# Kernel tuning notes

Hardware: AMD Instinct MI355X
Metric: run time of the kernel (lower is better)

The kernel has to match this reference:

```python
import jax, jax.numpy as jnp
import numpy as np

N_NODE = 100000
EMB = 112
NNZ = 1000000
B = 512
L = 50
LAYERS = 2


def setup_inputs() -> dict:
    key = jax.random.key(0)
    ks = jax.random.split(key, 9)
    embedding = jax.random.normal(ks[0], (N_NODE, EMB), dtype=jnp.float32) * 0.1
    adj_vals = jax.random.uniform(ks[1], (NNZ,), dtype=jnp.float32)
    adj_rows = jax.random.randint(ks[2], (NNZ,), 0, N_NODE, dtype=jnp.int32)
    adj_cols = jax.random.randint(ks[3], (NNZ,), 0, N_NODE, dtype=jnp.int32)
    D = jax.random.normal(ks[4], (B, B), dtype=jnp.float32) * (1.0 / B)
    A = jax.random.normal(ks[5], (B, B), dtype=jnp.float32)
    session_item = jax.random.randint(ks[6], (B, L), 0, N_NODE + 1, dtype=jnp.int32)  # 0 = pad row
    session_len = jnp.floor(jax.random.uniform(ks[7], (B, 1), dtype=jnp.float32) * (L - 1)) + 1.0
    stdv = 1.0 / np.sqrt(EMB)
    w_sess = jax.random.normal(ks[8], (LAYERS, EMB, EMB), dtype=jnp.float32) * stdv
    return {"embedding": embedding, "adj_vals": adj_vals, "adj_rows": adj_rows,
            "adj_cols": adj_cols, "D": D, "A": A, "session_item": session_item,
            "session_len": session_len, "w_sess": w_sess}


def _l2_normalize(x, eps=1e-12):
    n = jnp.linalg.norm(x, axis=-1, keepdims=True)
    return x / jnp.maximum(n, eps)


def _hyperconv(embedding, adj_vals, adj_rows, adj_cols):
    # mean over layer outputs of repeated sparse.mm(adjacency, embedding)
    cur = embedding
    acc = embedding
    for _ in range(LAYERS):
        msgs = adj_vals[:, None] * cur[adj_cols]           # [nnz, E] gather
        cur = jax.ops.segment_sum(msgs, adj_rows, num_segments=N_NODE)
        acc = acc + cur
    return acc / (LAYERS + 1)


def _sessconv(item_emb, D, A, session_item, session_len, w_sess):
    pad_emb = jnp.concatenate([jnp.zeros((1, EMB), item_emb.dtype), item_emb], axis=0)
    seq_h = pad_emb[session_item]                           # [B, L, E] gather (vectorized index_select loop)
    sess = jnp.sum(seq_h, axis=1) / session_len             # [B, E] mean pool
    DA = D @ A                                              # [B, B]
    acc = sess
    for i in range(LAYERS):
        sess = sess @ w_sess[i].T                           # Linear, no bias
        sess = DA @ sess
        sess = _l2_normalize(sess)
        acc = acc + sess
    return acc / (LAYERS + 1)


def reference(embedding, adj_vals, adj_rows, adj_cols, D, A, session_item, session_len, w_sess):
    item_emb = _hyperconv(embedding, adj_vals, adj_rows, adj_cols)
    sess_emb = _sessconv(item_emb, D, A, session_item, session_len, w_sess)
    return sess_emb
```

## Files before the change

### kernel.cpp

```cpp
#include <hip/hip_runtime.h>
#include <hip/hip_bf16.h>

#define N_NODE 100000
#define EMB 112
#define EMBQ 28
#define EMBQ4 14
#define EMBP4 16
#define EMBP2 32
#define NNZ 1000000
#define BATCH 512
#define SEQL 50

typedef unsigned int uint32;

__device__ __forceinline__ unsigned short f2bf(float f) {
    uint32 u = __float_as_uint(f);
    u = (u + 0x7fffu + ((u >> 16) & 1u)) >> 16;
    return (unsigned short)u;
}
__device__ __forceinline__ uint32 pack_bf2(float x, float y) {
    return (uint32)f2bf(x) | ((uint32)f2bf(y) << 16);
}
__device__ __forceinline__ float2 unpack_bf2(uint32 p) {
    float2 r;
    r.x = __uint_as_float(p << 16);
    r.y = __uint_as_float(p & 0xffff0000u);
    return r;
}

#define NPAD 100352
#define NBUCKET 196
#define BCAP 6144
#define CHUNK 2048
#define MS_BLOCKS 489
#define MAXC 25600
#define POISON ((int)0xAAAAAAAA)

__global__ __launch_bounds__(256)
void split_prep_kernel(const int* __restrict__ rows,
                       const int* __restrict__ cols,
                       const float* __restrict__ vals,
                       int* __restrict__ cur, int2* __restrict__ tmp,
                       const float4* __restrict__ embf4,
                       uint2* __restrict__ embb2,
                       const int* __restrict__ items,
                       int* __restrict__ flags, int* __restrict__ mapv,
                       int* __restrict__ rlist, int* __restrict__ cntp) {
    __shared__ int hist[NBUCKET];
    __shared__ int lexcl[NBUCKET];
    __shared__ int gbase[NBUCKET];
    __shared__ int lcur[NBUCKET];
    __shared__ int sscan[256];
    __shared__ unsigned char sbuck[CHUNK];
    __shared__ int2 stage[CHUNK];
    int t = threadIdx.x;
    if (blockIdx.x < MS_BLOCKS) {
        int base = blockIdx.x * CHUNK;
        int m = NNZ - base; if (m > CHUNK) m = CHUNK;
        for (int j = t; j < NBUCKET; j += 256) hist[j] = 0;
        __syncthreads();
        for (int i = t; i < m; i += 256) atomicAdd(&hist[rows[base + i] >> 9], 1);
        __syncthreads();
        int v = (t < NBUCKET) ? hist[t] : 0;
        sscan[t] = v;
        __syncthreads();
#pragma unroll
        for (int d = 1; d < 256; d <<= 1) {
            int x = (t >= d) ? sscan[t - d] : 0;
            __syncthreads();
            sscan[t] += x;
            __syncthreads();
        }
        if (t < NBUCKET) {
            int e = sscan[t] - v;
            lexcl[t] = e;
            lcur[t] = e;
            gbase[t] = t * BCAP + (atomicAdd(&cur[t], v) - POISON);
        }
        __syncthreads();
        for (int i = t; i < m; i += 256) {
            int r = rows[base + i];
            int b = r >> 9;
            int p = atomicAdd(&lcur[b], 1);
            stage[p] = make_int2(cols[base + i] | ((r & 511) << 17),
                                 __float_as_int(vals[base + i]));
            sbuck[p] = (unsigned char)b;
        }
        __syncthreads();
        for (int i = t; i < m; i += 256) {
            int b = sbuck[i];
            tmp[gbase[b] + (i - lexcl[b])] = stage[i];
        }
    } else {
        int i = (blockIdx.x - MS_BLOCKS) * 256 + t;
        if (i < N_NODE * EMBP2) {
            int row = i >> 5, u = i & 31;
            uint2 o;
            if (u < EMBQ) {
                float4 v = embf4[row * EMBQ + u];
                o.x = pack_bf2(v.x, v.y);
                o.y = pack_bf2(v.z, v.w);
            } else {
                o.x = 0u;
                o.y = 0u;
            }
            embb2[i] = o;
        }
        if (i < BATCH * SEQL) {
            int it = items[i];
            if (it > 0) {
                int old = atomicCAS(&flags[it - 1], POISON, 1);
                if (old == POISON) {
                    int rank = atomicAdd(cntp, 1) - POISON;
                    mapv[it - 1] = rank;
                    rlist[rank] = it - 1;
                }
            }
        }
    }
}

__global__ __launch_bounds__(256)
void sort_gemm_kernel(const int* __restrict__ cur, const int2* __restrict__ tmp,
                      int2* __restrict__ edges, int* __restrict__ off,
                      const float* __restrict__ D, const float* __restrict__ A,
                      float* __restrict__ DA) {
    __shared__ __align__(16) char smem[56320];
    int t = threadIdx.x;
    if (blockIdx.x < NBUCKET) {
        int* hist   = (int*)smem;
        int* scanb  = (int*)(smem + 2048);
        int* lcur   = (int*)(smem + 4096);
        int* sscan  = (int*)(smem + 6144);
        int2* stage = (int2*)(smem + 7168);
        int b = blockIdx.x;
        int base = b * BCAP;
        int cnt = cur[b] - POISON;
        for (int j = t; j < 512; j += 256) hist[j] = 0;
        __syncthreads();
        for (int i = t; i < cnt; i += 256) {
            int2 e = tmp[base + i];
            stage[i] = e;
            atomicAdd(&hist[(e.x >> 17) & 511], 1);
        }
        __syncthreads();
        int a0 = hist[2 * t], a1 = hist[2 * t + 1];
        int s = a0 + a1;
        sscan[t] = s;
        __syncthreads();
#pragma unroll
        for (int d = 1; d < 256; d <<= 1) {
            int x = (t >= d) ? sscan[t - d] : 0;
            __syncthreads();
            sscan[t] += x;
            __syncthreads();
        }
        int excl = sscan[t] - s;
        scanb[2 * t] = excl;
        scanb[2 * t + 1] = excl + a0;
        lcur[2 * t] = excl;
        lcur[2 * t + 1] = excl + a0;
        __syncthreads();
        for (int j = t; j < 512; j += 256) off[(b << 9) + j] = base + scanb[j];
        for (int i = t; i < cnt; i += 256) {
            int2 e = stage[i];
            int rl = (e.x >> 17) & 511;
            int p = atomicAdd(&lcur[rl], 1);
            edges[base + p] = make_int2(e.x & 0x1FFFF, e.y);
        }
    } else {
        float (*sDt)[36] = (float(*)[36])smem;
        float (*sA)[68] = (float(*)[68])(smem + 2304);
        int bx = blockIdx.x - NBUCKET;
        int tx = t & 15, ty = t >> 4;
        int m0 = (bx >> 3) * 32, n0 = (bx & 7) * 64;
        float acc[2][4];
#pragma unroll
        for (int i = 0; i < 2; ++i)
#pragma unroll
            for (int j = 0; j < 4; ++j) acc[i][j] = 0.0f;
        int dm = t >> 2, dk = (t & 3) * 4;
        int ak = t >> 4, an = (t & 15) * 4;
        for (int k0 = 0; k0 < BATCH; k0 += 16) {
            float4 dv;
            if (t < 128)
                dv = *(const float4*)(D + (size_t)(m0 + dm) * BATCH + k0 + dk);
            float4 av = *(const float4*)(A + (size_t)(k0 + ak) * BATCH + n0 + an);
            __syncthreads();
            if (t < 128) {
                sDt[dk + 0][dm] = dv.x;
                sDt[dk + 1][dm] = dv.y;
                sDt[dk + 2][dm] = dv.z;
                sDt[dk + 3][dm] = dv.w;
            }
            *(float4*)&sA[ak][an] = av;
            __syncthreads();
#pragma unroll
            for (int k = 0; k < 16; ++k) {
                float a0 = sDt[k][ty * 2 + 0];
                float a1 = sDt[k][ty * 2 + 1];
                float4 bv = *(const float4*)&sA[k][tx * 4];
                float br[4] = {bv.x, bv.y, bv.z, bv.w};
#pragma unroll
                for (int j = 0; j < 4; ++j) {
                    acc[0][j] += a0 * br[j];
                    acc[1][j] += a1 * br[j];
                }
            }
        }
#pragma unroll
        for (int i = 0; i < 2; ++i) {
            float4 o = make_float4(acc[i][0], acc[i][1], acc[i][2], acc[i][3]);
            *(float4*)(DA + (size_t)(m0 + ty * 2 + i) * BATCH + n0 + tx * 4) = o;
        }
    }
}

__global__ __launch_bounds__(256, 8)
void spmm_csr_kernel(const uint32* __restrict__ curb,
                     const float4* __restrict__ embf,
                     const int* __restrict__ rowptr,
                     const int* __restrict__ bcnt,
                     const int2* __restrict__ edges,
                     const int* __restrict__ rlist,
                     const int* __restrict__ cntp,
                     void* __restrict__ outm, int fuse_final) {
    int t = threadIdx.x;
    int lane16 = t & 15;
    int slot = t >> 4;
    int srcbase = t & 48;
    int idx = (blockIdx.x << 4) + slot;
    int r;
    if (rlist) {
        if (idx >= cntp[0] - POISON) return;
        r = rlist[idx];
    } else {
        r = idx;
        if (r >= N_NODE) return;
    }
    int beg = rowptr[r];
    int end = ((r & 511) == 511) ? ((r >> 9) * BCAP + (bcnt[r >> 9] - POISON))
                                 : rowptr[r + 1];
    int len = end - beg;
    int q = lane16;
    const uint4* basep = (const uint4*)curb;
    float4 accA = make_float4(0.0f, 0.0f, 0.0f, 0.0f);
    float4 accB = make_float4(0.0f, 0.0f, 0.0f, 0.0f);
    for (int b0 = 0; b0 < len; b0 += 16) {
        int m = len - b0; if (m > 16) m = 16;
        int2 e = (lane16 < m) ? edges[beg + b0 + lane16] : make_int2(0, 0);
        for (int k = 0; k < m; k += 4) {
            int   c0 = __shfl(e.x, srcbase + k + 0, 64);
            float v0 = __int_as_float(__shfl(e.y, srcbase + k + 0, 64));
            int   c1 = __shfl(e.x, srcbase + k + 1, 64);
            float v1 = __int_as_float(__shfl(e.y, srcbase + k + 1, 64));
            int   c2 = __shfl(e.x, srcbase + k + 2, 64);
            float v2 = __int_as_float(__shfl(e.y, srcbase + k + 2, 64));
            int   c3 = __shfl(e.x, srcbase + k + 3, 64);
            float v3 = __int_as_float(__shfl(e.y, srcbase + k + 3, 64));
            uint4 x0 = basep[(c0 << 4) + q];
            uint4 x1 = basep[(c1 << 4) + q];
            uint4 x2 = basep[(c2 << 4) + q];
            uint4 x3 = basep[(c3 << 4) + q];
            float2 p0a = unpack_bf2(x0.x), p0b = unpack_bf2(x0.y),
                   p0c = unpack_bf2(x0.z), p0d = unpack_bf2(x0.w);
            float2 p1a = unpack_bf2(x1.x), p1b = unpack_bf2(x1.y),
                   p1c = unpack_bf2(x1.z), p1d = unpack_bf2(x1.w);
            float2 p2a = unpack_bf2(x2.x), p2b = unpack_bf2(x2.y),
                   p2c = unpack_bf2(x2.z), p2d = unpack_bf2(x2.w);
            float2 p3a = unpack_bf2(x3.x), p3b = unpack_bf2(x3.y),
                   p3c = unpack_bf2(x3.z), p3d = unpack_bf2(x3.w);
            accA.x += v0 * p0a.x; accA.y += v0 * p0a.y;
            accA.z += v0 * p0b.x; accA.w += v0 * p0b.y;
            accB.x += v0 * p0c.x; accB.y += v0 * p0c.y;
            accB.z += v0 * p0d.x; accB.w += v0 * p0d.y;
            accA.x += v1 * p1a.x; accA.y += v1 * p1a.y;
            accA.z += v1 * p1b.x; accA.w += v1 * p1b.y;
            accB.x += v1 * p1c.x; accB.y += v1 * p1c.y;
            accB.z += v1 * p1d.x; accB.w += v1 * p1d.y;
            accA.x += v2 * p2a.x; accA.y += v2 * p2a.y;
            accA.z += v2 * p2b.x; accA.w += v2 * p2b.y;
            accB.x += v2 * p2c.x; accB.y += v2 * p2c.y;
            accB.z += v2 * p2d.x; accB.w += v2 * p2d.y;
            accA.x += v3 * p3a.x; accA.y += v3 * p3a.y;
            accA.z += v3 * p3b.x; accA.w += v3 * p3b.y;
            accB.x += v3 * p3c.x; accB.y += v3 * p3c.y;
            accB.z += v3 * p3d.x; accB.w += v3 * p3d.y;
        }
    }
    if (fuse_final) {
        if (q < EMBQ4) {
            uint4 cb = ((const uint4*)curb)[((size_t)r << 4) + q];
            float2 c0f = unpack_bf2(cb.x), c1f = unpack_bf2(cb.y),
                   c2f = unpack_bf2(cb.z), c3f = unpack_bf2(cb.w);
            float4 e0 = embf[(size_t)r * EMBQ + 2 * q];
            float4 e1 = embf[(size_t)r * EMBQ + 2 * q + 1];
            float4 r0, r1;
            r0.x = (accA.x + c0f.x + e0.x) * (1.0f / 3.0f);
            r0.y = (accA.y + c0f.y + e0.y) * (1.0f / 3.0f);
            r0.z = (accA.z + c1f.x + e0.z) * (1.0f / 3.0f);
            r0.w = (accA.w + c1f.y + e0.w) * (1.0f / 3.0f);
            r1.x = (accB.x + c2f.x + e1.x) * (1.0f / 3.0f);
            r1.y = (accB.y + c2f.y + e1.y) * (1.0f / 3.0f);
            r1.z = (accB.z + c3f.x + e1.z) * (1.0f / 3.0f);
            r1.w = (accB.w + c3f.y + e1.w) * (1.0f / 3.0f);
            ((float4*)outm)[(size_t)idx * EMBQ + 2 * q] = r0;
            ((float4*)outm)[(size_t)idx * EMBQ + 2 * q + 1] = r1;
        }
    } else {
        uint4 o4;
        o4.x = pack_bf2(accA.x, accA.y);
        o4.y = pack_bf2(accA.z, accA.w);
        o4.z = pack_bf2(accB.x, accB.y);
        o4.w = pack_bf2(accB.z, accB.w);
        ((uint4*)outm)[((size_t)r << 4) + q] = o4;
    }
}

__global__ __launch_bounds__(128)
void pool_lin_kernel(const float* __restrict__ item_c,
                     const int* __restrict__ map,
                     const int* __restrict__ items,
                     const float* __restrict__ slen,
                     const float* __restrict__ W1,
                     float* __restrict__ accb, float* __restrict__ t1) {
    __shared__ float srow[EMB];
    int b = blockIdx.x;
    int f = threadIdx.x;
    if (f < EMB) {
        float s = 0.0f;
        for (int l = 0; l < SEQL; ++l) {
            int it = items[b * SEQL + l];
            if (it > 0) s += item_c[(size_t)map[it - 1] * EMB + f];
        }
        s /= slen[b];
        srow[f] = s;
        accb[b * EMB + f] = s;
    }
    __syncthreads();
    if (f < EMB) {
        float a = 0.0f;
#pragma unroll 4
        for (int k = 0; k < EMB; ++k) a += srow[k] * W1[f * EMB + k];
        t1[b * EMB + f] = a;
    }
}

__global__ __launch_bounds__(128)
void damul_lin_kernel(const float* __restrict__ DA,
                      const float* __restrict__ t1,
                      const float* __restrict__ W2,
                      float* __restrict__ accb, float* __restrict__ t2) {
    __shared__ float srow[EMB];
    __shared__ float partial[2];
    int b = blockIdx.x;
    int j = threadIdx.x;
    float v = 0.0f;
    if (j < EMB) {
        const float* darow = DA + (size_t)b * BATCH;
        for (int k0 = 0; k0 < BATCH; k0 += 4) {
            float4 d4 = *(const float4*)(darow + k0);
            float a0 = t1[(k0 + 0) * EMB + j];
            float a1 = t1[(k0 + 1) * EMB + j];
            float a2 = t1[(k0 + 2) * EMB + j];
            float a3 = t1[(k0 + 3) * EMB + j];
            v += d4.x * a0 + d4.y * a1 + d4.z * a2 + d4.w * a3;
        }
    }
    float sq = (j < EMB) ? v * v : 0.0f;
#pragma unroll
    for (int off = 32; off > 0; off >>= 1) sq += __shfl_down(sq, off, 64);
    if ((j & 63) == 0) partial[j >> 6] = sq;
    __syncthreads();
    float inv = 1.0f / fmaxf(sqrtf(partial[0] + partial[1]), 1e-12f);
    if (j < EMB) {
        float s = v * inv;
        srow[j] = s;
        accb[b * EMB + j] += s;
    }
    __syncthreads();
    if (j < EMB) {
        float a = 0.0f;
#pragma unroll 4
        for (int k = 0; k < EMB; ++k) a += srow[k] * W2[j * EMB + k];
        t2[b * EMB + j] = a;
    }
}

__global__ __launch_bounds__(128)
void damul_out_kernel(const float* __restrict__ DA,
                      const float* __restrict__ t2,
                      const float* __restrict__ accb,
                      float* __restrict__ out) {
    __shared__ float partial[2];
    int b = blockIdx.x;
    int j = threadIdx.x;
    float v = 0.0f;
    if (j < EMB) {
        const float* darow = DA + (size_t)b * BATCH;
        for (int k0 = 0; k0 < BATCH; k0 += 4) {
            float4 d4 = *(const float4*)(darow + k0);
            float a0 = t2[(k0 + 0) * EMB + j];
            float a1 = t2[(k0 + 1) * EMB + j];
            float a2 = t2[(k0 + 2) * EMB + j];
            float a3 = t2[(k0 + 3) * EMB + j];
            v += d4.x * a0 + d4.y * a1 + d4.z * a2 + d4.w * a3;
        }
    }
    float sq = (j < EMB) ? v * v : 0.0f;
#pragma unroll
    for (int off = 32; off > 0; off >>= 1) sq += __shfl_down(sq, off, 64);
    if ((j & 63) == 0) partial[j >> 6] = sq;
    __syncthreads();
    float inv = 1.0f / fmaxf(sqrtf(partial[0] + partial[1]), 1e-12f);
    if (j < EMB) {
        float s = v * inv;
        out[b * EMB + j] = (accb[b * EMB + j] + s) * (1.0f / 3.0f);
    }
}

extern "C" void kernel_launch(void* const* d_in, const int* in_sizes, int n_in,
                              void* d_out, int out_size, void* d_ws, size_t ws_size,
                              hipStream_t stream) {
    const float* embedding = (const float*)d_in[0];
    const float* adj_vals  = (const float*)d_in[1];
    const int*   adj_rows  = (const int*)d_in[2];
    const int*   adj_cols  = (const int*)d_in[3];
    const float* D         = (const float*)d_in[4];
    const float* A         = (const float*)d_in[5];
    const int*   sess_item = (const int*)d_in[6];
    const float* sess_len  = (const float*)d_in[7];
    const float* w_sess    = (const float*)d_in[8];
    float* out = (float*)d_out;

    char* ws = (char*)d_ws;
    uint32* embb   = (uint32*)(ws);
    float*  item_c = (float*)(ws);
    uint32* next1b = (uint32*)(ws + 25600000);
    int2*   etmp   = (int2*)(ws + 25600000);
    int2*   edges  = (int2*)(ws + 51200000);
    int*    off    = (int*)(ws + 60833792);
    int*    mapv   = (int*)(ws + 61235200);
    int*    flags  = (int*)(ws + 61636608);
    int*    cntp   = (int*)(ws + 62038016);
    int*    curb   = (int*)(ws + 62038144);
    int*    rlist  = (int*)(ws + 62039168);
    float*  DA     = (float*)(ws + 62141568);
    float*  t1     = (float*)(ws + 63190144);
    float*  t2     = (float*)(ws + 63419520);
    float*  accb   = (float*)(ws + 63648896);


    {
        int conv_blocks = (N_NODE * EMBP2 + 255) / 256;
        split_prep_kernel<<<MS_BLOCKS + conv_blocks, 256, 0, stream>>>(
            adj_rows, adj_cols, adj_vals, curb, etmp,
            (const float4*)embedding, (uint2*)embb,
            sess_item, flags, mapv, rlist, cntp);
    }

    sort_gemm_kernel<<<NBUCKET + 128, 256, 0, stream>>>(curb, etmp, edges, off,
                                                        D, A, DA);

    {
        int grid1 = (N_NODE + 15) / 16;
        spmm_csr_kernel<<<grid1, 256, 0, stream>>>(embb, nullptr, off, curb,
                                                   edges, nullptr, nullptr,
                                                   next1b, 0);
        int grid2 = (MAXC + 15) / 16;
        spmm_csr_kernel<<<grid2, 256, 0, stream>>>(next1b, (const float4*)embedding,
                                                   off, curb, edges, rlist, cntp,
                                                   item_c, 1);
    }

    pool_lin_kernel<<<BATCH, 128, 0, stream>>>(item_c, mapv, sess_item, sess_len,
                                               w_sess, accb, t1);
    damul_lin_kernel<<<BATCH, 128, 0, stream>>>(DA, t1, w_sess + EMB * EMB,
                                                accb, t2);
    damul_out_kernel<<<BATCH, 128, 0, stream>>>(DA, t2, accb, out);
}
```

Measured before the change: 263.2 us.

## Fuse session pooling and DA layers into one persistent kernel with grid barriers

```diff
diff --git a/kernel.cpp b/kernel.cpp
--- a/kernel.cpp
+++ b/kernel.cpp
@@ -317,105 +317,149 @@
     }
 }
 
-__global__ __launch_bounds__(128)
-void pool_lin_kernel(const float* __restrict__ item_c,
-                     const int* __restrict__ map,
-                     const int* __restrict__ items,
-                     const float* __restrict__ slen,
-                     const float* __restrict__ W1,
-                     float* __restrict__ accb, float* __restrict__ t1) {
-    __shared__ float srow[EMB];
-    int b = blockIdx.x;
-    int f = threadIdx.x;
+#define FGRID 256
+__device__ __forceinline__ void grid_bar(int* p, int t) {
+    __threadfence();
+    __syncthreads();
+    if (t == 0) {
+        atomicAdd(p, 1);
+        while ((int)(__hip_atomic_load(p, __ATOMIC_ACQUIRE,
+                                       __HIP_MEMORY_SCOPE_AGENT) - POISON)
+               < FGRID) {
+            __builtin_amdgcn_s_sleep(2);
+        }
+        __threadfence();
+    }
+    __syncthreads();
+}
+
+#define KT 64
+__global__ __launch_bounds__(256)
+void sess_fused_kernel(const float* __restrict__ item_c,
+                       const int* __restrict__ map,
+                       const int* __restrict__ items,
+                       const float* __restrict__ slen,
+                       const float* __restrict__ w_sess,
+                       const float* __restrict__ DA,
+                       float* __restrict__ accb,
+                       float* __restrict__ t1,
+                       float* __restrict__ t2,
+                       float* __restrict__ out,
+                       int* __restrict__ bar) {
+    __shared__ __align__(16) char sm[30720];
+    float (*tile)[EMB]  = (float(*)[EMB])sm;
+    float (*daS)[KT]    = (float(*)[KT])(sm + 28672);
+    float* partial      = (float*)(sm + 29184);
+    float (*srow2)[EMB] = (float(*)[EMB])(sm + 29216);
+    int (*idxS)[SEQL]   = (int(*)[SEQL])(sm + 30112);
+    const float* W1 = w_sess;
+    const float* W2 = w_sess + EMB * EMB;
+
+    int b2 = blockIdx.x;
+    int t = threadIdx.x;
+    int row = t >> 7;
+    int f = t & 127;
+    int gr = b2 * 2 + row;
+
+    if (t < 2 * SEQL) {
+        int ss = t / SEQL, l = t - ss * SEQL;
+        int it = items[(b2 * 2 + ss) * SEQL + l];
+        idxS[ss][l] = (it > 0) ? map[it - 1] : -1;
+    }
+    __syncthreads();
     if (f < EMB) {
         float s = 0.0f;
+#pragma unroll 5
         for (int l = 0; l < SEQL; ++l) {
-            int it = items[b * SEQL + l];
-            if (it > 0) s += item_c[(size_t)map[it - 1] * EMB + f];
-        }
-        s /= slen[b];
-        srow[f] = s;
-        accb[b * EMB + f] = s;
+            int rr = idxS[row][l];
+            if (rr >= 0) s += item_c[(size_t)rr * EMB + f];
+        }
+        s /= slen[gr];
+        srow2[row][f] = s;
+        accb[gr * EMB + f] = s;
     }
     __syncthreads();
     if (f < EMB) {
         float a = 0.0f;
+        const float* w = W1 + (size_t)f * EMB;
 #pragma unroll 4
-        for (int k = 0; k < EMB; ++k) a += srow[k] * W1[f * EMB + k];
-        t1[b * EMB + f] = a;
-    }
-}
-
-__global__ __launch_bounds__(128)
-void damul_lin_kernel(const float* __restrict__ DA,
-                      const float* __restrict__ t1,
-                      const float* __restrict__ W2,
-                      float* __restrict__ accb, float* __restrict__ t2) {
-    __shared__ float srow[EMB];
-    __shared__ float partial[2];
-    int b = blockIdx.x;
-    int j = threadIdx.x;
-    float v = 0.0f;
-    if (j < EMB) {
-        const float* darow = DA + (size_t)b * BATCH;
-        for (int k0 = 0; k0 < BATCH; k0 += 4) {
-            float4 d4 = *(const float4*)(darow + k0);
-            float a0 = t1[(k0 + 0) * EMB + j];
-            float a1 = t1[(k0 + 1) * EMB + j];
-            float a2 = t1[(k0 + 2) * EMB + j];
-            float a3 = t1[(k0 + 3) * EMB + j];
-            v += d4.x * a0 + d4.y * a1 + d4.z * a2 + d4.w * a3;
-        }
-    }
-    float sq = (j < EMB) ? v * v : 0.0f;
-#pragma unroll
-    for (int off = 32; off > 0; off >>= 1) sq += __shfl_down(sq, off, 64);
-    if ((j & 63) == 0) partial[j >> 6] = sq;
-    __syncthreads();
-    float inv = 1.0f / fmaxf(sqrtf(partial[0] + partial[1]), 1e-12f);
-    if (j < EMB) {
-        float s = v * inv;
-        srow[j] = s;
-        accb[b * EMB + j] += s;
-    }
-    __syncthreads();
-    if (j < EMB) {
-        float a = 0.0f;
+        for (int k = 0; k < EMB; ++k) a += srow2[row][k] * w[k];
+        t1[gr * EMB + f] = a;
+    }
+    grid_bar(bar + 0, t);
+
+    {
+        float v = 0.0f;
+        for (int k0 = 0; k0 < BATCH; k0 += KT) {
+#pragma unroll
+            for (int i = t; i < KT * EMBQ; i += 256) {
+                int kk = i / EMBQ, c4 = i - kk * EMBQ;
+                *(float4*)&tile[kk][c4 * 4] =
+                    *(const float4*)&t1[(size_t)(k0 + kk) * EMB + c4 * 4];
+            }
+            if (t < 2 * KT)
+                daS[t >> 6][t & 63] =
+                    DA[(size_t)(b2 * 2 + (t >> 6)) * BATCH + k0 + (t & 63)];
+            __syncthreads();
+            if (f < EMB) {
+#pragma unroll 8
+                for (int kk = 0; kk < KT; ++kk) v += daS[row][kk] * tile[kk][f];
+            }
+            __syncthreads();
+        }
+        float sq = (f < EMB) ? v * v : 0.0f;
+#pragma unroll
+        for (int off = 32; off > 0; off >>= 1) sq += __shfl_down(sq, off, 64);
+        if ((t & 63) == 0) partial[t >> 6] = sq;
+        __syncthreads();
+        float inv = 1.0f / fmaxf(sqrtf(partial[row * 2] + partial[row * 2 + 1]),
+                                 1e-12f);
+        if (f < EMB) {
+            float sv = v * inv;
+            srow2[row][f] = sv;
+            accb[gr * EMB + f] += sv;
+        }
+        __syncthreads();
+        if (f < EMB) {
+            float a = 0.0f;
+            const float* w = W2 + (size_t)f * EMB;
 #pragma unroll 4
-        for (int k = 0; k < EMB; ++k) a += srow[k] * W2[j * EMB + k];
-        t2[b * EMB + j] = a;
-    }
-}
-
-__global__ __launch_bounds__(128)
-void damul_out_kernel(const float* __restrict__ DA,
-                      const float* __restrict__ t2,
-                      const float* __restrict__ accb,
-                      float* __restrict__ out) {
-    __shared__ float partial[2];
-    int b = blockIdx.x;
-    int j = threadIdx.x;
-    float v = 0.0f;
-    if (j < EMB) {
-        const float* darow = DA + (size_t)b * BATCH;
-        for (int k0 = 0; k0 < BATCH; k0 += 4) {
-            float4 d4 = *(const float4*)(darow + k0);
-            float a0 = t2[(k0 + 0) * EMB + j];
-            float a1 = t2[(k0 + 1) * EMB + j];
-            float a2 = t2[(k0 + 2) * EMB + j];
-            float a3 = t2[(k0 + 3) * EMB + j];
-            v += d4.x * a0 + d4.y * a1 + d4.z * a2 + d4.w * a3;
-        }
-    }
-    float sq = (j < EMB) ? v * v : 0.0f;
-#pragma unroll
-    for (int off = 32; off > 0; off >>= 1) sq += __shfl_down(sq, off, 64);
-    if ((j & 63) == 0) partial[j >> 6] = sq;
-    __syncthreads();
-    float inv = 1.0f / fmaxf(sqrtf(partial[0] + partial[1]), 1e-12f);
-    if (j < EMB) {
-        float s = v * inv;
-        out[b * EMB + j] = (accb[b * EMB + j] + s) * (1.0f / 3.0f);
+            for (int k = 0; k < EMB; ++k) a += srow2[row][k] * w[k];
+            t2[gr * EMB + f] = a;
+        }
+    }
+    grid_bar(bar + 1, t);
+
+    {
+        float v = 0.0f;
+        for (int k0 = 0; k0 < BATCH; k0 += KT) {
+#pragma unroll
+            for (int i = t; i < KT * EMBQ; i += 256) {
+                int kk = i / EMBQ, c4 = i - kk * EMBQ;
+                *(float4*)&tile[kk][c4 * 4] =
+                    *(const float4*)&t2[(size_t)(k0 + kk) * EMB + c4 * 4];
+            }
+            if (t < 2 * KT)
+                daS[t >> 6][t & 63] =
+                    DA[(size_t)(b2 * 2 + (t >> 6)) * BATCH + k0 + (t & 63)];
+            __syncthreads();
+            if (f < EMB) {
+#pragma unroll 8
+                for (int kk = 0; kk < KT; ++kk) v += daS[row][kk] * tile[kk][f];
+            }
+            __syncthreads();
+        }
+        float sq = (f < EMB) ? v * v : 0.0f;
+#pragma unroll
+        for (int off = 32; off > 0; off >>= 1) sq += __shfl_down(sq, off, 64);
+        if ((t & 63) == 0) partial[t >> 6] = sq;
+        __syncthreads();
+        float inv = 1.0f / fmaxf(sqrtf(partial[row * 2] + partial[row * 2 + 1]),
+                                 1e-12f);
+        if (f < EMB) {
+            float sv = v * inv;
+            out[gr * EMB + f] = (accb[gr * EMB + f] + sv) * (1.0f / 3.0f);
+        }
     }
 }
 
@@ -449,6 +493,7 @@
     float*  t1     = (float*)(ws + 63190144);
     float*  t2     = (float*)(ws + 63419520);
     float*  accb   = (float*)(ws + 63648896);
+    int*    bar    = (int*)(ws + 63878272);
 
 
     {
@@ -473,9 +518,7 @@
                                                    item_c, 1);
     }
 
-    pool_lin_kernel<<<BATCH, 128, 0, stream>>>(item_c, mapv, sess_item, sess_len,
-                                               w_sess, accb, t1);
-    damul_lin_kernel<<<BATCH, 128, 0, stream>>>(DA, t1, w_sess + EMB * EMB,
-                                                accb, t2);
-    damul_out_kernel<<<BATCH, 128, 0, stream>>>(DA, t2, accb, out);
-}
+    sess_fused_kernel<<<FGRID, 256, 0, stream>>>(item_c, mapv, sess_item,
+                                                 sess_len, w_sess, DA, accb,
+                                                 t1, t2, out, bar);
+}
```

New measurement: 320.5 us. 1.22x slower.

## Process two session rows per block in pooling and DA-multiply kernels

Applied to the files above, without the earlier changes.

```diff
diff --git a/kernel.cpp b/kernel.cpp
--- a/kernel.cpp
+++ b/kernel.cpp
@@ -317,105 +317,112 @@
     }
 }
 
-__global__ __launch_bounds__(128)
-void pool_lin_kernel(const float* __restrict__ item_c,
-                     const int* __restrict__ map,
-                     const int* __restrict__ items,
-                     const float* __restrict__ slen,
-                     const float* __restrict__ W1,
-                     float* __restrict__ accb, float* __restrict__ t1) {
-    __shared__ float srow[EMB];
-    int b = blockIdx.x;
-    int f = threadIdx.x;
-    if (f < EMB) {
+__global__ __launch_bounds__(256)
+void pool_lin2_kernel(const float* __restrict__ item_c,
+                      const int* __restrict__ map,
+                      const int* __restrict__ items,
+                      const float* __restrict__ slen,
+                      const float* __restrict__ W1,
+                      float* __restrict__ accb, float* __restrict__ t1) {
+    __shared__ float srow[2][EMB];
+    __shared__ int idxS[2][SEQL];
+    int t = threadIdx.x, b2 = blockIdx.x;
+    int row = t >> 7, j = t & 127;
+    int gr = b2 * 2 + row;
+    if (t < 2 * SEQL) {
+        int ss = t / SEQL, l = t - ss * SEQL;
+        int it = items[(b2 * 2 + ss) * SEQL + l];
+        idxS[ss][l] = (it > 0) ? map[it - 1] : -1;
+    }
+    __syncthreads();
+    if (j < EMB) {
         float s = 0.0f;
+#pragma unroll 10
         for (int l = 0; l < SEQL; ++l) {
-            int it = items[b * SEQL + l];
-            if (it > 0) s += item_c[(size_t)map[it - 1] * EMB + f];
-        }
-        s /= slen[b];
-        srow[f] = s;
-        accb[b * EMB + f] = s;
-    }
-    __syncthreads();
-    if (f < EMB) {
-        float a = 0.0f;
-#pragma unroll 4
-        for (int k = 0; k < EMB; ++k) a += srow[k] * W1[f * EMB + k];
-        t1[b * EMB + f] = a;
-    }
-}
-
-__global__ __launch_bounds__(128)
-void damul_lin_kernel(const float* __restrict__ DA,
-                      const float* __restrict__ t1,
-                      const float* __restrict__ W2,
-                      float* __restrict__ accb, float* __restrict__ t2) {
-    __shared__ float srow[EMB];
-    __shared__ float partial[2];
-    int b = blockIdx.x;
-    int j = threadIdx.x;
-    float v = 0.0f;
-    if (j < EMB) {
-        const float* darow = DA + (size_t)b * BATCH;
-        for (int k0 = 0; k0 < BATCH; k0 += 4) {
-            float4 d4 = *(const float4*)(darow + k0);
-            float a0 = t1[(k0 + 0) * EMB + j];
-            float a1 = t1[(k0 + 1) * EMB + j];
-            float a2 = t1[(k0 + 2) * EMB + j];
-            float a3 = t1[(k0 + 3) * EMB + j];
-            v += d4.x * a0 + d4.y * a1 + d4.z * a2 + d4.w * a3;
-        }
-    }
-    float sq = (j < EMB) ? v * v : 0.0f;
-#pragma unroll
-    for (int off = 32; off > 0; off >>= 1) sq += __shfl_down(sq, off, 64);
-    if ((j & 63) == 0) partial[j >> 6] = sq;
-    __syncthreads();
-    float inv = 1.0f / fmaxf(sqrtf(partial[0] + partial[1]), 1e-12f);
-    if (j < EMB) {
-        float s = v * inv;
-        srow[j] = s;
-        accb[b * EMB + j] += s;
+            int rr = idxS[row][l];
+            int rc = rr < 0 ? 0 : rr;
+            float x = item_c[(size_t)rc * EMB + j];
+            s += (rr >= 0) ? x : 0.0f;
+        }
+        s /= slen[gr];
+        srow[row][j] = s;
+        accb[gr * EMB + j] = s;
     }
     __syncthreads();
     if (j < EMB) {
         float a = 0.0f;
-#pragma unroll 4
-        for (int k = 0; k < EMB; ++k) a += srow[k] * W2[j * EMB + k];
-        t2[b * EMB + j] = a;
-    }
-}
-
-__global__ __launch_bounds__(128)
-void damul_out_kernel(const float* __restrict__ DA,
-                      const float* __restrict__ t2,
-                      const float* __restrict__ accb,
-                      float* __restrict__ out) {
+        const float* w = W1 + (size_t)j * EMB;
+#pragma unroll 8
+        for (int k = 0; k < EMB; ++k) a += srow[row][k] * w[k];
+        t1[gr * EMB + j] = a;
+    }
+}
+
+__global__ __launch_bounds__(256, 4)
+void damul2_kernel(const float* __restrict__ DA,
+                   const float* __restrict__ tin,
+                   const float* __restrict__ W2,
+                   float* __restrict__ accb,
+                   float* __restrict__ tout,
+                   float* __restrict__ outp, int final_mode) {
+    __shared__ float daS[2][BATCH];
+    __shared__ float srow[2][EMB];
     __shared__ float partial[2];
-    int b = blockIdx.x;
-    int j = threadIdx.x;
-    float v = 0.0f;
-    if (j < EMB) {
-        const float* darow = DA + (size_t)b * BATCH;
-        for (int k0 = 0; k0 < BATCH; k0 += 4) {
-            float4 d4 = *(const float4*)(darow + k0);
-            float a0 = t2[(k0 + 0) * EMB + j];
-            float a1 = t2[(k0 + 1) * EMB + j];
-            float a2 = t2[(k0 + 2) * EMB + j];
-            float a3 = t2[(k0 + 3) * EMB + j];
-            v += d4.x * a0 + d4.y * a1 + d4.z * a2 + d4.w * a3;
-        }
-    }
-    float sq = (j < EMB) ? v * v : 0.0f;
-#pragma unroll
-    for (int off = 32; off > 0; off >>= 1) sq += __shfl_down(sq, off, 64);
-    if ((j & 63) == 0) partial[j >> 6] = sq;
+    int t = threadIdx.x, b2 = blockIdx.x;
+    int row = t >> 7, j = t & 127;
+    int gr = b2 * 2 + row;
+    {
+        int ss = t >> 7, c = t & 127;
+        *(float4*)&daS[ss][c * 4] =
+            *(const float4*)&DA[(size_t)(b2 * 2 + ss) * BATCH + c * 4];
+    }
     __syncthreads();
-    float inv = 1.0f / fmaxf(sqrtf(partial[0] + partial[1]), 1e-12f);
-    if (j < EMB) {
-        float s = v * inv;
-        out[b * EMB + j] = (accb[b * EMB + j] + s) * (1.0f / 3.0f);
+    float4 v4 = make_float4(0.0f, 0.0f, 0.0f, 0.0f);
+    if (j < EMBQ) {
+        const float4* t4 = (const float4*)tin;
+        for (int k = 0; k < BATCH; k += 16) {
+#pragma unroll
+            for (int u = 0; u < 16; ++u) {
+                float da = daS[row][k + u];
+                float4 x = t4[(size_t)(k + u) * EMBQ + j];
+                v4.x += da * x.x; v4.y += da * x.y;
+                v4.z += da * x.z; v4.w += da * x.w;
+            }
+        }
+    }
+    float sq = v4.x * v4.x + v4.y * v4.y + v4.z * v4.z + v4.w * v4.w;
+#pragma unroll
+    for (int off = 16; off > 0; off >>= 1) sq += __shfl_down(sq, off, 32);
+    if (j == 0) partial[row] = sq;
+    __syncthreads();
+    float inv = 1.0f / fmaxf(sqrtf(partial[row]), 1e-12f);
+    if (j < EMBQ) {
+        float4 s4;
+        s4.x = v4.x * inv; s4.y = v4.y * inv;
+        s4.z = v4.z * inv; s4.w = v4.w * inv;
+        float4 ab = *(const float4*)&accb[(size_t)gr * EMB + j * 4];
+        if (final_mode) {
+            float4 o;
+            o.x = (ab.x + s4.x) * (1.0f / 3.0f);
+            o.y = (ab.y + s4.y) * (1.0f / 3.0f);
+            o.z = (ab.z + s4.z) * (1.0f / 3.0f);
+            o.w = (ab.w + s4.w) * (1.0f / 3.0f);
+            *(float4*)&outp[(size_t)gr * EMB + j * 4] = o;
+        } else {
+            *(float4*)&srow[row][j * 4] = s4;
+            ab.x += s4.x; ab.y += s4.y; ab.z += s4.z; ab.w += s4.w;
+            *(float4*)&accb[(size_t)gr * EMB + j * 4] = ab;
+        }
+    }
+    if (!final_mode) {
+        __syncthreads();
+        if (j < EMB) {
+            float a = 0.0f;
+            const float* w = W2 + (size_t)j * EMB;
+#pragma unroll 8
+            for (int k = 0; k < EMB; ++k) a += srow[row][k] * w[k];
+            tout[gr * EMB + j] = a;
+        }
     }
 }
 
@@ -473,9 +480,10 @@
                                                    item_c, 1);
     }
 
-    pool_lin_kernel<<<BATCH, 128, 0, stream>>>(item_c, mapv, sess_item, sess_len,
-                                               w_sess, accb, t1);
-    damul_lin_kernel<<<BATCH, 128, 0, stream>>>(DA, t1, w_sess + EMB * EMB,
-                                                accb, t2);
-    damul_out_kernel<<<BATCH, 128, 0, stream>>>(DA, t2, accb, out);
-}
+    pool_lin2_kernel<<<BATCH / 2, 256, 0, stream>>>(item_c, mapv, sess_item,
+                                                    sess_len, w_sess, accb, t1);
+    damul2_kernel<<<BATCH / 2, 256, 0, stream>>>(DA, t1, w_sess + EMB * EMB,
+                                                 accb, t2, nullptr, 0);
+    damul2_kernel<<<BATCH / 2, 256, 0, stream>>>(DA, t2, w_sess, accb,
+                                                 t1, out, 1);
+}
```

Result: faster. 255.9 us (-2.8%).
